# Performance work log

Hardware: AMD Instinct MI355X
Metric: run time of the kernel (lower is better)

The kernel has to match this reference:

```python
import jax, jax.numpy as jnp
import numpy as np

NUM_HEADS = 4
LN_EPS = 1e-5
L2_EPS = 1e-12


def setup_inputs() -> dict:
    key = jax.random.key(0)
    ks = jax.random.split(key, 10)
    B, L, D, Hd = 256, 197, 768, 512
    dh = Hd // NUM_HEADS  # 128
    NC = 1000
    sc = lambda k, shape, s: jax.random.normal(k, shape, jnp.float32) * s
    return {
        "cls_token": jax.random.normal(ks[0], (B, D), jnp.float32),
        "x": jax.random.normal(ks[1], (B, L, D), jnp.float32),
        "proj_w": sc(ks[2], (D, Hd), 0.02),
        "proj_b": jnp.zeros((Hd,), jnp.float32),
        "ln_g": jnp.ones((dh,), jnp.float32),
        "ln_b": jnp.zeros((dh,), jnp.float32),
        "conv1_w": sc(ks[3], (3, 3, 3, 3), 0.2),
        "conv2_w": sc(ks[4], (3, 3, 3, 3), 0.2),
        "cls1_w": sc(ks[5], (D, NC), 0.02),
        "cls1_b": jnp.zeros((NC,), jnp.float32),
        "cls2_w": sc(ks[6], (2883, NC), 0.02),
        "cls2_b": jnp.zeros((NC,), jnp.float32),
    }


def reference(cls_token, x, proj_w, proj_b, ln_g, ln_b, conv1_w, conv2_w,
              cls1_w, cls1_b, cls2_w, cls2_b):
    B, L, D = x.shape
    dh = ln_g.shape[0]
    # proj on patch tokens (drop cls at position 0)
    xp = x[:, 1:, :] @ proj_w + proj_b            # (B, 196, 512)
    Lp = xp.shape[1]
    H = xp.shape[2] // dh
    heads = xp.reshape(B, Lp, H, dh).transpose(2, 0, 1, 3)  # (H, B, Lp, dh)
    # LayerNorm over last dim (eps=1e-5, biased var, affine)
    mu = heads.mean(-1, keepdims=True)
    var = heads.var(-1, keepdims=True)
    hn = (heads - mu) * jax.lax.rsqrt(var + LN_EPS) * ln_g + ln_b
    # Covariance._remove_mean: adaptive_avg_pool2d on (B, dh, Lp) -> mean over BOTH dh and Lp per sample
    hn = hn - hn.mean(axis=(2, 3), keepdims=True)
    # 'near' cross-covariances between adjacent heads, all pairs batched
    x1, x2 = hn[:-1], hn[1:]                      # (H-1, B, Lp, dh)
    cov = jnp.einsum('pbnd,pbne->pbde', x1, x2) / Lp  # (H-1, B, dh, dh)
    # L2 normalize over dim=2 (row axis of each dh x dh map), F.normalize eps
    nrm = jnp.sqrt(jnp.sum(cov * cov, axis=2, keepdims=True))
    cov = cov / jnp.maximum(nrm, L2_EPS)
    cov = cov.transpose(1, 0, 2, 3)               # (B, 3, 128, 128)
    conv = lambda z, w: jax.lax.conv_general_dilated(
        z, w, (2, 2), 'VALID', dimension_numbers=('NCHW', 'OIHW', 'NCHW'))
    z = conv(cov, conv1_w)                        # (B, 3, 63, 63)
    z = jax.nn.gelu(z, approximate=False)
    z = conv(z, conv2_w)                          # (B, 3, 31, 31)
    flat = z.reshape(B, -1)                       # (B, 2883)
    out = ((cls_token @ cls1_w + cls1_b) + (flat @ cls2_w + cls2_b)) / 2
    return out
```

## Files before the change

### kernel.cpp

```cpp
#include <hip/hip_runtime.h>
#include <hip/hip_bf16.h>
#include <cstdint>

typedef __bf16 bf16_t;
typedef __bf16 bf16x4 __attribute__((ext_vector_type(4)));
typedef __bf16 bf16x8 __attribute__((ext_vector_type(8)));
typedef float floatx4 __attribute__((ext_vector_type(4)));
typedef unsigned int u32;
typedef unsigned short ushort8 __attribute__((ext_vector_type(8)));
typedef unsigned int u32x2 __attribute__((ext_vector_type(2)));

#define LNEPS 1e-5f

__device__ inline void async_copy16(const bf16_t* g, bf16_t* l) {
    __builtin_amdgcn_global_load_lds((const __attribute__((address_space(1))) void*)g,
                                     (__attribute__((address_space(3))) void*)l,
                                     16, 0, 0);
}

__global__ __launch_bounds__(256)
void k_prep(const float* __restrict__ x,   bf16_t* __restrict__ xbf,
            const float* __restrict__ w,   bf16_t* __restrict__ wt,
            const float* __restrict__ cls, bf16_t* __restrict__ Xb,
            float* __restrict__ csum,
            const float* __restrict__ W1,  const float* __restrict__ W2,
            bf16_t* __restrict__ Wb)
{
    __shared__ bf16_t tile[32][33];
    const int bid = blockIdx.x;
    const int t = threadIdx.x;

    if (bid < 18816) {
        const int vid = bid * 256 + t;
        const int row = vid / 96;
        const int kv  = vid - row * 96;
        const int b = row / 196, l = row - (row / 196) * 196;
        const float* src = x + ((b * 197 + l + 1) * 96 + kv) * 8;
        const floatx4 f0 = *(const floatx4*)src;
        const floatx4 f1 = *(const floatx4*)(src + 4);
        bf16x8 o;
#pragma unroll
        for (int e = 0; e < 4; e++) { o[e] = (bf16_t)f0[e]; o[e+4] = (bf16_t)f1[e]; }
        *(bf16x8*)(xbf + vid * 8) = o;
    } else if (bid < 19200) {
        const int id = bid - 18816;
        const int bx = id & 15;
        const int by = id >> 4;
        const int tx = t & 31, ty = t >> 5;
        for (int i = ty; i < 32; i += 8)
            tile[i][tx] = (bf16_t)w[(by*32 + i)*512 + bx*32 + tx];
        __syncthreads();
        for (int i = ty; i < 32; i += 8)
            wt[(bx*32 + i)*768 + by*32 + tx] = tile[tx][i];
    } else if (bid < 19456) {
        const int b = bid - 19200;
        for (int k = t; k < 768; k += 256)
            Xb[b*3712 + k] = (bf16_t)cls[b*768 + k];
        if (t < 61) Xb[b*3712 + 3651 + t] = (bf16_t)0.f;
        float* cz = csum + b*512;
        cz[t] = 0.f; cz[t + 256] = 0.f;
    } else {
        const int id = bid - 19456;
        const int k0 = (id % 116) * 32;
        const int n0 = (id / 116) * 32;
        const int tx = t & 31, ty = t >> 5;
        for (int i = ty; i < 32; i += 8) {
            const int k = k0 + i, n = n0 + tx;
            float v = 0.f;
            if (n < 1000 && k < 3651)
                v = (k < 768) ? W1[k*1000 + n] : W2[(k-768)*1000 + n];
            tile[i][tx] = (bf16_t)v;
        }
        __syncthreads();
        for (int i = ty; i < 32; i += 8)
            Wb[(n0 + i)*3712 + k0 + tx] = tile[tx][i];
    }
}

__global__ __launch_bounds__(256, 3)
void k_proj_ln(const bf16_t* __restrict__ xbf, const bf16_t* __restrict__ wt,
               const float* __restrict__ pb, const float* __restrict__ lng,
               const float* __restrict__ lnb, bf16_t* __restrict__ hn,
               float* __restrict__ csum)
{
    __shared__ bf16_t As[3][128*32];
    __shared__ bf16_t Bs[3][128*32];

    const int t = threadIdx.x;
    const int lane = t & 63;
    const int wv = t >> 6;
    const int q = lane >> 4;
    const int c = lane & 15;
    const int L = blockIdx.x;
    const int xcd = L & 7, slot = L >> 3;
    const int h = slot & 3;
    const int m0 = (xcd + 8 * (slot >> 2)) * 128;

    const int srow  = t >> 2;
    const int skoff = (t & 3) * 8;
    const bf16_t* ag = xbf + (m0 + srow) * 768 + skoff;
    const bf16_t* bg = wt + (h*128 + srow) * 768 + skoff;

#define STAGE(B, kk)                                                     \
    {                                                                    \
        const int kn_ = (kk) * 32;                                       \
        async_copy16(ag + kn_,          &As[B][t*8]);                    \
        async_copy16(ag + 64*768 + kn_, &As[B][2048 + t*8]);             \
        async_copy16(bg + kn_,          &Bs[B][t*8]);                    \
        async_copy16(bg + 64*768 + kn_, &Bs[B][2048 + t*8]);             \
    }

#define COMPUTE(B)                                                       \
    {                                                                    \
        bf16x8 af[2], bfr[8];                                            \
        _Pragma("unroll")                                                \
        for (int i = 0; i < 2; i++)                                      \
            af[i] = *(const bf16x8*)&As[B][(wv*32 + i*16 + c)*32 + q*8]; \
        _Pragma("unroll")                                                \
        for (int j = 0; j < 8; j++)                                      \
            bfr[j] = *(const bf16x8*)&Bs[B][(j*16 + c)*32 + q*8];        \
        _Pragma("unroll")                                                \
        for (int i = 0; i < 2; i++)                                      \
            _Pragma("unroll")                                            \
            for (int j = 0; j < 8; j++)                                  \
                acc[i][j] = __builtin_amdgcn_mfma_f32_16x16x32_bf16(af[i], bfr[j], acc[i][j], 0, 0, 0); \
    }

    floatx4 acc[2][8];
#pragma unroll
    for (int i = 0; i < 2; i++)
#pragma unroll
        for (int j = 0; j < 8; j++)
#pragma unroll
            for (int r = 0; r < 4; r++) acc[i][j][r] = 0.f;

    STAGE(0, 0);
    STAGE(1, 1);
    STAGE(2, 2);

    for (int ks = 0; ks < 22; ks++) {
        const int buf = ks % 3;
        asm volatile("s_waitcnt vmcnt(8)" ::: "memory");
        __builtin_amdgcn_s_barrier();
        COMPUTE(buf);
        __builtin_amdgcn_s_barrier();
        if (ks < 21) STAGE(buf, ks + 3);
    }
    asm volatile("s_waitcnt vmcnt(4)" ::: "memory");
    __builtin_amdgcn_s_barrier();
    COMPUTE(1);
    __builtin_amdgcn_s_barrier();
    asm volatile("s_waitcnt vmcnt(0)" ::: "memory");
    __builtin_amdgcn_s_barrier();
    COMPUTE(2);

#undef STAGE
#undef COMPUTE

    float bias[8], gg[8], bb[8];
#pragma unroll
    for (int j = 0; j < 8; j++) {
        const int d = j*16 + c;
        bias[j] = pb[h*128 + d];
        gg[j]   = lng[d];
        bb[j]   = lnb[d];
    }
    float cs0[8], cs1[8];
#pragma unroll
    for (int j = 0; j < 8; j++) { cs0[j] = 0.f; cs1[j] = 0.f; }
    const int b0 = m0 / 196;
    const int bL = (m0 + 127) / 196;
#pragma unroll
    for (int i = 0; i < 2; i++) {
#pragma unroll
        for (int r = 0; r < 4; r++) {
            float s = 0.f, s2 = 0.f;
#pragma unroll
            for (int j = 0; j < 8; j++) {
                const float v = acc[i][j][r] + bias[j];
                acc[i][j][r] = v;
                s += v; s2 += v*v;
            }
#pragma unroll
            for (int o = 1; o < 16; o <<= 1) { s += __shfl_xor(s, o); s2 += __shfl_xor(s2, o); }
            const float mu = s * (1.f/128.f);
            const float ms = s2 * (1.f/128.f);
            const float rstd = rsqrtf(ms - mu*mu + LNEPS);
            const int gm = m0 + wv*32 + i*16 + q*4 + r;
            const int bI = gm / 196, l = gm - bI*196;
            bf16_t* dst = hn + (((h*256 + bI)*196 + l) << 7);
            const bool first = (bI == b0);
#pragma unroll
            for (int j = 0; j < 8; j++) {
                const float v = (acc[i][j][r] - mu)*rstd*gg[j] + bb[j];
                dst[j*16 + c] = (bf16_t)v;
                cs0[j] += first ? v : 0.f;
                cs1[j] += first ? 0.f : v;
            }
        }
    }
    float* scr = (float*)As;
#pragma unroll
    for (int j = 0; j < 8; j++) {
        float s0 = cs0[j], s1 = cs1[j];
        s0 += __shfl_xor(s0, 16); s0 += __shfl_xor(s0, 32);
        s1 += __shfl_xor(s1, 16); s1 += __shfl_xor(s1, 32);
        if (q == 0) {
            scr[(wv*2 + 0)*128 + j*16 + c] = s0;
            scr[(wv*2 + 1)*128 + j*16 + c] = s1;
        }
    }
    __syncthreads();
    {
        const int bucket = t >> 7, d = t & 127;
        if (bucket == 0 || bL > b0) {
            const float s = scr[(0*2 + bucket)*128 + d] + scr[(1*2 + bucket)*128 + d]
                          + scr[(2*2 + bucket)*128 + d] + scr[(3*2 + bucket)*128 + d];
            atomicAdd(&csum[((h*256 + b0 + bucket) << 7) + d], s);
        }
    }
}

__global__ __launch_bounds__(256, 3)
void k_cov(const bf16_t* __restrict__ hn, const float* __restrict__ colsum,
           float* __restrict__ cov)
{
    __shared__ u32 x1s[128*18];
    __shared__ u32 x2s[128*18];
    __shared__ float rs1[128], rs2[128];
    __shared__ float colsq[2][128];
    __shared__ float nrm_inv[128];
    __shared__ float mu_s[2];

    const int t = threadIdx.x;
    const int lane = t & 63;
    const int wv = t >> 6;
    const int wr = wv >> 1, wc = wv & 1;
    const int q = lane >> 4;
    const int c = lane & 15;
    const int b = blockIdx.x;
    const int p = blockIdx.y;

    const bf16_t* X1 = hn + (((p*256 + b)*196) << 7);
    const bf16_t* X2 = hn + ((((p+1)*256 + b)*196) << 7);

    if (t < 128) rs1[t] = colsum[((p*256 + b) << 7) + t];
    else         rs2[t & 127] = colsum[(((p+1)*256 + b) << 7) + (t & 127)];
    __syncthreads();
    if (wv == 0) {
        float s = rs1[lane] + rs1[lane + 64];
#pragma unroll
        for (int o = 1; o < 64; o <<= 1) s += __shfl_xor(s, o);
        if (lane == 0) mu_s[0] = s * (1.f/(196.f*128.f));
    } else if (wv == 1) {
        float s = rs2[lane] + rs2[lane + 64];
#pragma unroll
        for (int o = 1; o < 64; o <<= 1) s += __shfl_xor(s, o);
        if (lane == 0) mu_s[1] = s * (1.f/(196.f*128.f));
    }

    floatx4 acc[4][4];
#pragma unroll
    for (int i = 0; i < 4; i++)
#pragma unroll
        for (int j = 0; j < 4; j++)
#pragma unroll
            for (int r = 0; r < 4; r++) acc[i][j][r] = 0.f;

    const int np  = t & 15;
    const int dch = t >> 4;

    ushort8 cva, cvb, cwa, cwb;
    {
        const int na = 2*np, nb = na + 1;
        cva = *(const ushort8*)(X1 + (na << 7) + dch*8);
        cwa = *(const ushort8*)(X2 + (na << 7) + dch*8);
        cvb = *(const ushort8*)(X1 + (nb << 7) + dch*8);
        cwb = *(const ushort8*)(X2 + (nb << 7) + dch*8);
    }

    for (int n0 = 0; n0 < 224; n0 += 32) {
        __syncthreads();
#pragma unroll
        for (int e = 0; e < 8; e++) {
            x1s[(dch*8 + e)*18 + np] = (u32)cva[e] | ((u32)cvb[e] << 16);
            x2s[(dch*8 + e)*18 + np] = (u32)cwa[e] | ((u32)cwb[e] << 16);
        }
        __syncthreads();
        if (n0 + 32 < 224) {
            const int na = n0 + 32 + 2*np, nb = na + 1;
            ushort8 z;
#pragma unroll
            for (int e = 0; e < 8; e++) z[e] = 0;
            ushort8 nva = z, nvb = z, nwa = z, nwb = z;
            if (na < 196) {
                nva = *(const ushort8*)(X1 + (na << 7) + dch*8);
                nwa = *(const ushort8*)(X2 + (na << 7) + dch*8);
            }
            if (nb < 196) {
                nvb = *(const ushort8*)(X1 + (nb << 7) + dch*8);
                nwb = *(const ushort8*)(X2 + (nb << 7) + dch*8);
            }
            cva = nva; cvb = nvb; cwa = nwa; cwb = nwb;
        }
        bf16x8 af[4], bfr[4];
#pragma unroll
        for (int i = 0; i < 4; i++) {
            const int base = (wr*64 + i*16 + c)*18 + q*4;
            u32 tmp[4];
            *(u32x2*)&tmp[0] = *(const u32x2*)&x1s[base];
            *(u32x2*)&tmp[2] = *(const u32x2*)&x1s[base + 2];
            __builtin_memcpy(&af[i], tmp, 16);
        }
#pragma unroll
        for (int j = 0; j < 4; j++) {
            const int base = (wc*64 + j*16 + c)*18 + q*4;
            u32 tmp[4];
            *(u32x2*)&tmp[0] = *(const u32x2*)&x2s[base];
            *(u32x2*)&tmp[2] = *(const u32x2*)&x2s[base + 2];
            __builtin_memcpy(&bfr[j], tmp, 16);
        }
#pragma unroll
        for (int i = 0; i < 4; i++)
#pragma unroll
            for (int j = 0; j < 4; j++)
                acc[i][j] = __builtin_amdgcn_mfma_f32_16x16x32_bf16(af[i], bfr[j], acc[i][j], 0, 0, 0);
    }

    const float mu1 = mu_s[0], mu2 = mu_s[1];
    const float invL = 1.f/196.f;
    float csq[4] = {0.f, 0.f, 0.f, 0.f};
#pragma unroll
    for (int i = 0; i < 4; i++)
#pragma unroll
        for (int j = 0; j < 4; j++)
#pragma unroll
            for (int r = 0; r < 4; r++) {
                const int d = wr*64 + i*16 + q*4 + r;
                const int e = wc*64 + j*16 + c;
                const float v = acc[i][j][r]*invL - mu2*rs1[d]*invL - mu1*rs2[e]*invL + mu1*mu2;
                acc[i][j][r] = v;
                csq[j] += v*v;
            }
#pragma unroll
    for (int j = 0; j < 4; j++) {
        float s = csq[j];
        s += __shfl_xor(s, 16);
        s += __shfl_xor(s, 32);
        csq[j] = s;
    }
    if (q == 0) {
#pragma unroll
        for (int j = 0; j < 4; j++) colsq[wr][wc*64 + j*16 + c] = csq[j];
    }
    __syncthreads();
    if (t < 128) {
        const float nr = sqrtf(colsq[0][t] + colsq[1][t]);
        nrm_inv[t] = 1.f / fmaxf(nr, 1e-12f);
    }
    __syncthreads();
    float* dst = cov + ((long)b*3 + p)*16384;
#pragma unroll
    for (int i = 0; i < 4; i++)
#pragma unroll
        for (int j = 0; j < 4; j++) {
            const int e = wc*64 + j*16 + c;
            const float ni = nrm_inv[e];
#pragma unroll
            for (int r = 0; r < 4; r++) {
                const int d = wr*64 + i*16 + q*4 + r;
                dst[(d << 7) + e] = acc[i][j][r] * ni;
            }
        }
}

__global__ __launch_bounds__(256)
void k_convs(const float* __restrict__ cov, const float* __restrict__ w1,
             const float* __restrict__ w2, bf16_t* __restrict__ Xb)
{
    __shared__ float Z[3*33*63];
    __shared__ float W1s[81];
    __shared__ float W2s[81];
    const int t = threadIdx.x;
    const int b = blockIdx.x >> 1, half = blockIdx.x & 1;
    const int zy0 = half ? 32 : 0;
    const int nzy = half ? 31 : 33;
    const int y20 = half ? 16 : 0;
    const int ny2 = half ? 15 : 16;
    if (t < 81) { W1s[t] = w1[t]; W2s[t] = w2[t]; }
    __syncthreads();
    const float* C = cov + (long)b*3*16384;
    const int ztot = 3*nzy*63;
    for (int idx = t; idx < ztot; idx += 256) {
        const int o = idx / (nzy*63), rem = idx - o*(nzy*63);
        const int yl = rem / 63, xx = rem - yl*63;
        const int y = zy0 + yl;
        float a = 0.f;
#pragma unroll
        for (int i = 0; i < 3; i++) {
            const float* Ci = C + i*16384 + (2*y)*128 + 2*xx;
            const float* Wi = &W1s[o*27 + i*9];
            a += Ci[0]*Wi[0]   + Ci[1]*Wi[1]   + Ci[2]*Wi[2]
               + Ci[128]*Wi[3] + Ci[129]*Wi[4] + Ci[130]*Wi[5]
               + Ci[256]*Wi[6] + Ci[257]*Wi[7] + Ci[258]*Wi[8];
        }
        Z[o*2079 + yl*63 + xx] = 0.5f*a*(1.0f + erff(a*0.70710678118654752f));
    }
    __syncthreads();
    const int c2tot = 3*ny2*31;
    for (int idx = t; idx < c2tot; idx += 256) {
        const int o = idx / (ny2*31), rem = idx - o*(ny2*31);
        const int y2l = rem / 31, x2 = rem - y2l*31;
        float a = 0.f;
#pragma unroll
        for (int i = 0; i < 3; i++) {
            const float* Zi = Z + i*2079 + (2*y2l)*63 + 2*x2;
            const float* Wi = &W2s[(o*3+i)*9];
            a += Zi[0]*Wi[0]   + Zi[1]*Wi[1]   + Zi[2]*Wi[2]
               + Zi[63]*Wi[3]  + Zi[64]*Wi[4]  + Zi[65]*Wi[5]
               + Zi[126]*Wi[6] + Zi[127]*Wi[7] + Zi[128]*Wi[8];
        }
        const int oy2 = y20 + y2l;
        Xb[(long)b*3712 + 768 + o*961 + oy2*31 + x2] = (bf16_t)a;
    }
}

__global__ __launch_bounds__(256, 2)
void k_gemm_cls(const bf16_t* __restrict__ Xb, const bf16_t* __restrict__ Wb,
                float* __restrict__ partial)
{
    __shared__ bf16_t As[3][128*32];
    __shared__ bf16_t Bs[3][128*32];

    const int t = threadIdx.x;
    const int lane = t & 63;
    const int wv = t >> 6;
    const int wr = wv >> 1, wc = wv & 1;
    const int q = lane >> 4;
    const int c = lane & 15;
    const int nt = blockIdx.x;
    const int mt = blockIdx.y;
    const int sp = blockIdx.z;

    const int srow  = t >> 2;
    const int skoff = (t & 3) * 8;
    const int m0 = mt * 128, n0 = nt * 128;
    const int kbase = sp * 928;
    const bf16_t* ag0 = Xb + (m0 + srow) * 3712 + kbase + skoff;
    const bf16_t* ag1 = Xb + (m0 + srow + 64) * 3712 + kbase + skoff;
    const bf16_t* bg0 = Wb + (n0 + srow) * 3712 + kbase + skoff;
    const bf16_t* bg1 = Wb + (n0 + srow + 64) * 3712 + kbase + skoff;

#define GSTAGE(B, kk)                                                    \
    {                                                                    \
        const int kn_ = (kk) * 32;                                       \
        async_copy16(ag0 + kn_, &As[B][t*8]);                            \
        async_copy16(ag1 + kn_, &As[B][2048 + t*8]);                     \
        async_copy16(bg0 + kn_, &Bs[B][t*8]);                            \
        async_copy16(bg1 + kn_, &Bs[B][2048 + t*8]);                     \
    }

#define GCOMPUTE(B)                                                      \
    {                                                                    \
        bf16x8 af[4], bfr[4];                                            \
        _Pragma("unroll")                                                \
        for (int i = 0; i < 4; i++)                                      \
            af[i] = *(const bf16x8*)&As[B][(wr*64 + i*16 + c)*32 + q*8]; \
        _Pragma("unroll")                                                \
        for (int j = 0; j < 4; j++)                                      \
            bfr[j] = *(const bf16x8*)&Bs[B][(wc*64 + j*16 + c)*32 + q*8];\
        _Pragma("unroll")                                                \
        for (int i = 0; i < 4; i++)                                      \
            _Pragma("unroll")                                            \
            for (int j = 0; j < 4; j++)                                  \
                acc[i][j] = __builtin_amdgcn_mfma_f32_16x16x32_bf16(af[i], bfr[j], acc[i][j], 0, 0, 0); \
    }

    floatx4 acc[4][4];
#pragma unroll
    for (int i = 0; i < 4; i++)
#pragma unroll
        for (int j = 0; j < 4; j++)
#pragma unroll
            for (int r = 0; r < 4; r++) acc[i][j][r] = 0.f;

    GSTAGE(0, 0);
    GSTAGE(1, 1);
    GSTAGE(2, 2);

    for (int ks = 0; ks < 27; ks++) {
        const int buf = ks % 3;
        asm volatile("s_waitcnt vmcnt(8)" ::: "memory");
        __builtin_amdgcn_s_barrier();
        GCOMPUTE(buf);
        __builtin_amdgcn_s_barrier();
        if (ks < 26) GSTAGE(buf, ks + 3);
    }
    asm volatile("s_waitcnt vmcnt(4)" ::: "memory");
    __builtin_amdgcn_s_barrier();
    GCOMPUTE(0);
    __builtin_amdgcn_s_barrier();
    asm volatile("s_waitcnt vmcnt(0)" ::: "memory");
    __builtin_amdgcn_s_barrier();
    GCOMPUTE(1);

#undef GSTAGE
#undef GCOMPUTE

    float* base = partial + ((long)sp*256 + m0)*1024 + n0;
#pragma unroll
    for (int i = 0; i < 4; i++)
#pragma unroll
        for (int r = 0; r < 4; r++) {
            const int row = wr*64 + i*16 + q*4 + r;
#pragma unroll
            for (int j = 0; j < 4; j++)
                base[row*1024 + wc*64 + j*16 + c] = acc[i][j][r];
        }
}

__global__ __launch_bounds__(256)
void k_cls_fin(const float* __restrict__ partial, const float* __restrict__ b1,
               const float* __restrict__ b2, float* __restrict__ out)
{
    const int idx = blockIdx.x * 256 + threadIdx.x;
    const int m = idx / 1000, n = idx - m*1000;
    float s = partial[(m)*1024 + n] + partial[(256 + m)*1024 + n]
            + partial[(512 + m)*1024 + n] + partial[(768 + m)*1024 + n];
    out[idx] = 0.5f*(s + b1[n] + b2[n]);
}

extern "C" void kernel_launch(void* const* d_in, const int* in_sizes, int n_in,
                              void* d_out, int out_size, void* d_ws, size_t ws_size,
                              hipStream_t stream) {
    const float* cls = (const float*)d_in[0];
    const float* x   = (const float*)d_in[1];
    const float* pw  = (const float*)d_in[2];
    const float* pb  = (const float*)d_in[3];
    const float* lng = (const float*)d_in[4];
    const float* lnb = (const float*)d_in[5];
    const float* c1w = (const float*)d_in[6];
    const float* c2w = (const float*)d_in[7];
    const float* w1  = (const float*)d_in[8];
    const float* b1  = (const float*)d_in[9];
    const float* w2  = (const float*)d_in[10];
    const float* b2  = (const float*)d_in[11];

    char* ws = (char*)d_ws;
    bf16_t* hn    = (bf16_t*)(ws);
    bf16_t* xbf   = (bf16_t*)(ws + 51380224ull);
    float*  covb  = (float*) (ws + 51380224ull);
    bf16_t* wt    = (bf16_t*)(ws + 128450560ull);
    float*  csum  = (float*) (ws + 129236992ull);
    bf16_t* Xb    = (bf16_t*)(ws + 129761280ull);
    bf16_t* Wb    = (bf16_t*)(ws + 131661824ull);
    float*  part  = (float*) (ws + 139264000ull);
    float*  out   = (float*)d_out;

    k_prep<<<23168, 256, 0, stream>>>(x, xbf, pw, wt, cls, Xb, csum, w1, w2, Wb);
    k_proj_ln<<<1568, 256, 0, stream>>>(xbf, wt, pb, lng, lnb, hn, csum);
    k_cov<<<dim3(256, 3), 256, 0, stream>>>(hn, csum, covb);
    k_convs<<<512, 256, 0, stream>>>(covb, c1w, c2w, Xb);
    k_gemm_cls<<<dim3(8, 2, 4), 256, 0, stream>>>(Xb, Wb, part);
    k_cls_fin<<<1000, 256, 0, stream>>>(part, b1, b2, out);
}
```

Baseline: 401.1 us.

## Enlarge proj+LN GEMM tile to 256 rows per block and drop XCD swizzle

Doubles the M-tile of the projection GEMM from 128 to 256 rows, so each wave computes 64 rows and each staged weight tile is reused across twice as many rows. The grid is halved to 784 blocks, the column-sum buckets grow to three per block, and the XCD-aware block remapping becomes a simple linear mapping. The cost is more accumulator registers and LDS, with occupancy lowered to 2 blocks per CU, and possibly worse L2 locality across XCDs.

```diff
diff --git a/kernel.cpp b/kernel.cpp
--- a/kernel.cpp
+++ b/kernel.cpp
@@ -77,13 +77,13 @@
     }
 }
 
-__global__ __launch_bounds__(256, 3)
+__global__ __launch_bounds__(256, 2)
 void k_proj_ln(const bf16_t* __restrict__ xbf, const bf16_t* __restrict__ wt,
                const float* __restrict__ pb, const float* __restrict__ lng,
                const float* __restrict__ lnb, bf16_t* __restrict__ hn,
                float* __restrict__ csum)
 {
-    __shared__ bf16_t As[3][128*32];
+    __shared__ bf16_t As[3][256*32];
     __shared__ bf16_t Bs[3][128*32];
 
     const int t = threadIdx.x;
@@ -91,44 +91,48 @@
     const int wv = t >> 6;
     const int q = lane >> 4;
     const int c = lane & 15;
-    const int L = blockIdx.x;
-    const int xcd = L & 7, slot = L >> 3;
-    const int h = slot & 3;
-    const int m0 = (xcd + 8 * (slot >> 2)) * 128;
+    const int h  = blockIdx.x & 3;
+    const int m0 = (blockIdx.x >> 2) * 256;
 
     const int srow  = t >> 2;
     const int skoff = (t & 3) * 8;
-    const bf16_t* ag = xbf + (m0 + srow) * 768 + skoff;
-    const bf16_t* bg = wt + (h*128 + srow) * 768 + skoff;
+    const bf16_t* ag0 = xbf + (size_t)(m0 + srow) * 768 + skoff;
+    const bf16_t* ag1 = ag0 +  64*768;
+    const bf16_t* ag2 = ag0 + 128*768;
+    const bf16_t* ag3 = ag0 + 192*768;
+    const bf16_t* bg  = wt + (h*128 + srow) * 768 + skoff;
+    const bf16_t* bg2 = bg + 64*768;
 
 #define STAGE(B, kk)                                                     \
     {                                                                    \
         const int kn_ = (kk) * 32;                                       \
-        async_copy16(ag + kn_,          &As[B][t*8]);                    \
-        async_copy16(ag + 64*768 + kn_, &As[B][2048 + t*8]);             \
-        async_copy16(bg + kn_,          &Bs[B][t*8]);                    \
-        async_copy16(bg + 64*768 + kn_, &Bs[B][2048 + t*8]);             \
+        async_copy16(ag0 + kn_, &As[B][t*8]);                            \
+        async_copy16(ag1 + kn_, &As[B][2048 + t*8]);                     \
+        async_copy16(ag2 + kn_, &As[B][4096 + t*8]);                     \
+        async_copy16(ag3 + kn_, &As[B][6144 + t*8]);                     \
+        async_copy16(bg  + kn_, &Bs[B][t*8]);                            \
+        async_copy16(bg2 + kn_, &Bs[B][2048 + t*8]);                     \
     }
 
 #define COMPUTE(B)                                                       \
     {                                                                    \
-        bf16x8 af[2], bfr[8];                                            \
+        bf16x8 af[4], bfr[8];                                            \
         _Pragma("unroll")                                                \
-        for (int i = 0; i < 2; i++)                                      \
-            af[i] = *(const bf16x8*)&As[B][(wv*32 + i*16 + c)*32 + q*8]; \
+        for (int i = 0; i < 4; i++)                                      \
+            af[i] = *(const bf16x8*)&As[B][(wv*64 + i*16 + c)*32 + q*8]; \
         _Pragma("unroll")                                                \
         for (int j = 0; j < 8; j++)                                      \
             bfr[j] = *(const bf16x8*)&Bs[B][(j*16 + c)*32 + q*8];        \
         _Pragma("unroll")                                                \
-        for (int i = 0; i < 2; i++)                                      \
+        for (int i = 0; i < 4; i++)                                      \
             _Pragma("unroll")                                            \
             for (int j = 0; j < 8; j++)                                  \
                 acc[i][j] = __builtin_amdgcn_mfma_f32_16x16x32_bf16(af[i], bfr[j], acc[i][j], 0, 0, 0); \
     }
 
-    floatx4 acc[2][8];
-#pragma unroll
-    for (int i = 0; i < 2; i++)
+    floatx4 acc[4][8];
+#pragma unroll
+    for (int i = 0; i < 4; i++)
 #pragma unroll
         for (int j = 0; j < 8; j++)
 #pragma unroll
@@ -140,13 +144,13 @@
 
     for (int ks = 0; ks < 22; ks++) {
         const int buf = ks % 3;
-        asm volatile("s_waitcnt vmcnt(8)" ::: "memory");
+        asm volatile("s_waitcnt vmcnt(12)" ::: "memory");
         __builtin_amdgcn_s_barrier();
         COMPUTE(buf);
         __builtin_amdgcn_s_barrier();
         if (ks < 21) STAGE(buf, ks + 3);
     }
-    asm volatile("s_waitcnt vmcnt(4)" ::: "memory");
+    asm volatile("s_waitcnt vmcnt(6)" ::: "memory");
     __builtin_amdgcn_s_barrier();
     COMPUTE(1);
     __builtin_amdgcn_s_barrier();
@@ -165,13 +169,13 @@
         gg[j]   = lng[d];
         bb[j]   = lnb[d];
     }
-    float cs0[8], cs1[8];
-#pragma unroll
-    for (int j = 0; j < 8; j++) { cs0[j] = 0.f; cs1[j] = 0.f; }
+    float cs0[8], cs1[8], cs2[8];
+#pragma unroll
+    for (int j = 0; j < 8; j++) { cs0[j] = 0.f; cs1[j] = 0.f; cs2[j] = 0.f; }
     const int b0 = m0 / 196;
-    const int bL = (m0 + 127) / 196;
-#pragma unroll
-    for (int i = 0; i < 2; i++) {
+    const int bL = (m0 + 255) / 196;
+#pragma unroll
+    for (int i = 0; i < 4; i++) {
 #pragma unroll
         for (int r = 0; r < 4; r++) {
             float s = 0.f, s2 = 0.f;
@@ -186,37 +190,43 @@
             const float mu = s * (1.f/128.f);
             const float ms = s2 * (1.f/128.f);
             const float rstd = rsqrtf(ms - mu*mu + LNEPS);
-            const int gm = m0 + wv*32 + i*16 + q*4 + r;
+            const int gm = m0 + wv*64 + i*16 + q*4 + r;
             const int bI = gm / 196, l = gm - bI*196;
             bf16_t* dst = hn + (((h*256 + bI)*196 + l) << 7);
-            const bool first = (bI == b0);
+            const int bk = bI - b0;
 #pragma unroll
             for (int j = 0; j < 8; j++) {
                 const float v = (acc[i][j][r] - mu)*rstd*gg[j] + bb[j];
                 dst[j*16 + c] = (bf16_t)v;
-                cs0[j] += first ? v : 0.f;
-                cs1[j] += first ? 0.f : v;
+                cs0[j] += (bk == 0) ? v : 0.f;
+                cs1[j] += (bk == 1) ? v : 0.f;
+                cs2[j] += (bk == 2) ? v : 0.f;
             }
         }
     }
     float* scr = (float*)As;
 #pragma unroll
     for (int j = 0; j < 8; j++) {
-        float s0 = cs0[j], s1 = cs1[j];
+        float s0 = cs0[j], s1 = cs1[j], s2 = cs2[j];
         s0 += __shfl_xor(s0, 16); s0 += __shfl_xor(s0, 32);
         s1 += __shfl_xor(s1, 16); s1 += __shfl_xor(s1, 32);
+        s2 += __shfl_xor(s2, 16); s2 += __shfl_xor(s2, 32);
         if (q == 0) {
-            scr[(wv*2 + 0)*128 + j*16 + c] = s0;
-            scr[(wv*2 + 1)*128 + j*16 + c] = s1;
+            scr[(wv*3 + 0)*128 + j*16 + c] = s0;
+            scr[(wv*3 + 1)*128 + j*16 + c] = s1;
+            scr[(wv*3 + 2)*128 + j*16 + c] = s2;
         }
     }
     __syncthreads();
-    {
-        const int bucket = t >> 7, d = t & 127;
-        if (bucket == 0 || bL > b0) {
-            const float s = scr[(0*2 + bucket)*128 + d] + scr[(1*2 + bucket)*128 + d]
-                          + scr[(2*2 + bucket)*128 + d] + scr[(3*2 + bucket)*128 + d];
-            atomicAdd(&csum[((h*256 + b0 + bucket) << 7) + d], s);
+    if (t < 128) {
+        const int d = t;
+#pragma unroll
+        for (int bucket = 0; bucket < 3; bucket++) {
+            if (bucket <= bL - b0) {
+                const float s = scr[(0*3 + bucket)*128 + d] + scr[(1*3 + bucket)*128 + d]
+                              + scr[(2*3 + bucket)*128 + d] + scr[(3*3 + bucket)*128 + d];
+                atomicAdd(&csum[((h*256 + b0 + bucket) << 7) + d], s);
+            }
         }
     }
 }
@@ -558,7 +568,7 @@
     float*  out   = (float*)d_out;
 
     k_prep<<<23168, 256, 0, stream>>>(x, xbf, pw, wt, cls, Xb, csum, w1, w2, Wb);
-    k_proj_ln<<<1568, 256, 0, stream>>>(xbf, wt, pb, lng, lnb, hn, csum);
+    k_proj_ln<<<784, 256, 0, stream>>>(xbf, wt, pb, lng, lnb, hn, csum);
     k_cov<<<dim3(256, 3), 256, 0, stream>>>(hn, csum, covb);
     k_convs<<<512, 256, 0, stream>>>(covb, c1w, c2w, Xb);
     k_gemm_cls<<<dim3(8, 2, 4), 256, 0, stream>>>(Xb, Wb, part);
```

After: 406.6 us. No clear change (+1.4%).
